# Performance work log

Measured on AMD Instinct MI355X. Metric: run time of the kernel, lower is better.

Reference implementation:

```python
import jax, jax.numpy as jnp
import numpy as np

B, S, H = 4, 4096, 768
NB = 16            # n_blocks (first factor)
BSZ = H // NB      # 48, block size
LN_EPS = 1e-12


def setup_inputs() -> dict:
    key = jax.random.key(0)
    ks = jax.random.split(key, 6)
    hidden_states = jax.random.normal(ks[0], (B, S, H), dtype=jnp.float32)
    # Monarch factors: B1 has NB blocks of (BSZ,BSZ); B2 has BSZ blocks of (NB,NB)
    w1_blocks = jax.random.normal(ks[1], (NB, BSZ, BSZ), dtype=jnp.float32) / np.sqrt(BSZ)
    w2_blocks = jax.random.normal(ks[2], (BSZ, NB, NB), dtype=jnp.float32) / np.sqrt(NB)
    gate_w = jax.random.normal(ks[3], (H, H), dtype=jnp.float32) / np.sqrt(H)
    gate_b = jnp.zeros((H,), dtype=jnp.float32)
    out_w = jax.random.normal(ks[4], (H, H), dtype=jnp.float32) / np.sqrt(H)
    out_b = jnp.zeros((H,), dtype=jnp.float32)
    ln_gamma = jnp.ones((H,), dtype=jnp.float32)
    ln_beta = jnp.zeros((H,), dtype=jnp.float32)
    return {
        "hidden_states": hidden_states,
        "w1_blocks": w1_blocks,
        "w2_blocks": w2_blocks,
        "gate_w": gate_w,
        "gate_b": gate_b,
        "out_w": out_w,
        "out_b": out_b,
        "ln_gamma": ln_gamma,
        "ln_beta": ln_beta,
    }


def _monarch(x, w1, w2):
    # x: [B, S, H]; Monarch product P B2 P B1 applied to last dim.
    b, s, h = x.shape
    y = x.reshape(b, s, NB, BSZ)
    y = jnp.einsum('bski,kij->bskj', y, w1)      # block-diag (NB blocks of BSZxBSZ)
    y = jnp.swapaxes(y, -1, -2)                  # permute: [B,S,BSZ,NB]
    y = jnp.einsum('bsqi,qij->bsqj', y, w2)      # block-diag (BSZ blocks of NBxNB)
    y = jnp.swapaxes(y, -1, -2)                  # permute back: [B,S,NB,BSZ]
    return y.reshape(b, s, h)


def _layernorm(x, gamma, beta, eps):
    mu = jnp.mean(x, axis=-1, keepdims=True)
    var = jnp.mean(jnp.square(x - mu), axis=-1, keepdims=True)
    return (x - mu) * jax.lax.rsqrt(var + eps) * gamma + beta


def reference(hidden_states, w1_blocks, w2_blocks, gate_w, gate_b,
              out_w, out_b, ln_gamma, ln_beta):
    residual = hidden_states
    mixed = _monarch(hidden_states, w1_blocks, w2_blocks)
    gate = jax.nn.sigmoid(hidden_states @ gate_w.T + gate_b)
    h = mixed * gate
    h = h @ out_w.T + out_b
    # dropout is identity in eval / p=0
    return _layernorm(h + residual, ln_gamma, ln_beta, LN_EPS)
```

## Files before the change

kernel.cpp:

```cpp
#include <hip/hip_runtime.h>
#include <hip/hip_bf16.h>
#include <stdint.h>

#define HD 768

typedef __attribute__((ext_vector_type(8))) short bf16x8;
typedef __attribute__((ext_vector_type(4))) float f32x4;

typedef __attribute__((address_space(3))) void lds_void_t;
typedef const __attribute__((address_space(1))) void gbl_void_t;

__device__ inline void gload_lds16(const void* g, void* l) {
  __builtin_amdgcn_global_load_lds((gbl_void_t*)g, (lds_void_t*)l, 16, 0, 0);
}

__device__ inline unsigned short f2bf(float f) {
  union { float f; unsigned int u; } v; v.f = f;
  return (unsigned short)((v.u + 0x7fffu + ((v.u >> 16) & 1u)) >> 16);
}
__device__ inline float bf2f(unsigned short u) {
  union { unsigned int uu; float f; } v; v.uu = ((unsigned int)u) << 16;
  return v.f;
}

#define BAR() asm volatile("s_barrier" ::: "memory")
#define LGKM(N) { asm volatile("s_waitcnt lgkmcnt(" #N ")" ::: "memory"); __builtin_amdgcn_sched_barrier(0); }
#define VMC(N) asm volatile("s_waitcnt vmcnt(" #N ")" ::: "memory")

__global__ void prep_all_kernel(const float* __restrict__ x,
                                const float* __restrict__ gw, const float* __restrict__ ow,
                                const float* __restrict__ w1, const float* __restrict__ w2,
                                unsigned short* __restrict__ xb,
                                unsigned short* __restrict__ Gwb, unsigned short* __restrict__ Lwb,
                                unsigned short* __restrict__ Opk) {
  int bid = blockIdx.x;
  if (bid < 12288) {
    int i = bid * 256 + threadIdx.x;
    float4 v = ((const float4*)x)[i];
    ushort4 o;
    o.x = f2bf(v.x); o.y = f2bf(v.y); o.z = f2bf(v.z); o.w = f2bf(v.w);
    ((ushort4*)xb)[i] = o;
  } else if (bid < 14592) {
    int e = (bid - 12288) * 256 + threadIdx.x;
    Gwb[e] = f2bf(gw[e]);
  } else if (bid < 16896) {
    int e = (bid - 14592) * 256 + threadIdx.x;
    int n = e / 768, m = e - (e / 768) * 768;
    int k = n / 48, q = n - k * 48;
    int i2 = m / 48, ii = m - i2 * 48;
    float v = w1[(i2 * 48 + ii) * 48 + q] * w2[(q * 16 + i2) * 16 + k];
    Lwb[e] = f2bf(v);
  } else {
    int r = (bid - 16896) * 256 + threadIdx.x;
    int lane = r & 63;
    int ks = (r >> 6) % 24;
    int nt = r / (24 * 64);
    int n = nt * 16 + (lane & 15);
    int k = ks * 32 + (lane >> 4) * 8;
    bf16x8 pack;
#pragma unroll
    for (int j = 0; j < 8; ++j) pack[j] = (short)f2bf(ow[(size_t)n * HD + k + j]);
    *(bf16x8*)(Opk + (size_t)r * 8) = pack;
  }
}

__global__ __launch_bounds__(256, 2)
void gatemix_kernel(const unsigned short* __restrict__ xb,
                    const unsigned short* __restrict__ Gwb,
                    const unsigned short* __restrict__ Lwb,
                    const float* __restrict__ gate_b,
                    unsigned short* __restrict__ hb) {
  __shared__ __align__(16) unsigned char lds[81920];
  const int tid = threadIdx.x, lane = tid & 63;
  const int wid = tid >> 6, wm = wid >> 1, wn = wid & 1;
  const int lr = lane & 15, lg = lane >> 4;

  const int b = blockIdx.x;
  const int work = (b & 7) * 128 + (b >> 3);
  const int panel = work >> 3, nwin = work & 7;
  const size_t m0 = (size_t)panel * 128;
  const int n0 = nwin * 96;

  const int r0 = tid >> 3;
  const int sw = ((tid & 7) << 4) ^ ((r0 & 7) << 4);
  const int v0 = (0 * 32 + r0) * 1536 + sw;
  const int v1 = (1 * 32 + r0) * 1536 + sw;
  const int v2 = (2 * 32 + r0) * 1536 + sw;
  const int v3 = (3 * 32 + r0) * 1536 + sw;
  const unsigned char* aS = (const unsigned char*)xb + m0 * 1536;
  const unsigned char* gS = (const unsigned char*)Gwb + (size_t)n0 * 1536;
  const unsigned char* lS = (const unsigned char*)Lwb + (size_t)n0 * 1536;

#define STAGE_A(KT, BUF) { const unsigned char* s = aS + (KT) * 128; \
    gload_lds16(s + v0, lds + (BUF) * 16384 + tid * 16); \
    gload_lds16(s + v1, lds + (BUF) * 16384 + 4096 + tid * 16); \
    gload_lds16(s + v2, lds + (BUF) * 16384 + 8192 + tid * 16); \
    gload_lds16(s + v3, lds + (BUF) * 16384 + 12288 + tid * 16); }
#define STAGE_BG(KT, BUF) { const unsigned char* s = gS + (KT) * 128; \
    gload_lds16(s + v0, lds + 32768 + (BUF) * 12288 + tid * 16); \
    gload_lds16(s + v1, lds + 32768 + (BUF) * 12288 + 4096 + tid * 16); \
    gload_lds16(s + v2, lds + 32768 + (BUF) * 12288 + 8192 + tid * 16); }
#define STAGE_BL(KT, BUF) { const unsigned char* s = lS + (KT) * 128; \
    gload_lds16(s + v0, lds + 57344 + (BUF) * 12288 + tid * 16); \
    gload_lds16(s + v1, lds + 57344 + (BUF) * 12288 + 4096 + tid * 16); \
    gload_lds16(s + v2, lds + 57344 + (BUF) * 12288 + 8192 + tid * 16); }

  const int sx0 = (lg * 16) ^ ((lr & 7) << 4);
  const int sx1 = sx0 ^ 64;
  const unsigned char* baA0 = lds + (wm * 64 + lr) * 128 + sx0;
  const unsigned char* baA1 = lds + (wm * 64 + lr) * 128 + sx1;
  const unsigned char* baG0 = lds + 32768 + (wn * 48 + lr) * 128 + sx0;
  const unsigned char* baG1 = lds + 32768 + (wn * 48 + lr) * 128 + sx1;
  const unsigned char* baL0 = lds + 57344 + (wn * 48 + lr) * 128 + sx0;
  const unsigned char* baL1 = lds + 57344 + (wn * 48 + lr) * 128 + sx1;

  f32x4 accg[4][3], accm[4][3];
#pragma unroll
  for (int mt = 0; mt < 4; ++mt)
#pragma unroll
    for (int nt = 0; nt < 3; ++nt) { accg[mt][nt] = (f32x4){0,0,0,0}; accm[mt][nt] = (f32x4){0,0,0,0}; }

  bf16x8 aA[4], aB[4];
  bf16x8 bG[3], bL[3];

#define RD_AA(BUF) { _Pragma("unroll") for (int mt = 0; mt < 4; ++mt) \
      aA[mt] = *(const bf16x8*)(baA0 + (BUF) * 16384 + mt * 2048); }
#define RD_AB(BUF) { _Pragma("unroll") for (int mt = 0; mt < 4; ++mt) \
      aB[mt] = *(const bf16x8*)(baA1 + (BUF) * 16384 + mt * 2048); }
#define RD_BG0(BUF) { _Pragma("unroll") for (int nt = 0; nt < 3; ++nt) \
      bG[nt] = *(const bf16x8*)(baG0 + (BUF) * 12288 + nt * 2048); }
#define RD_BG1(BUF) { _Pragma("unroll") for (int nt = 0; nt < 3; ++nt) \
      bG[nt] = *(const bf16x8*)(baG1 + (BUF) * 12288 + nt * 2048); }
#define RD_BL0(BUF) { _Pragma("unroll") for (int nt = 0; nt < 3; ++nt) \
      bL[nt] = *(const bf16x8*)(baL0 + (BUF) * 12288 + nt * 2048); }
#define RD_BL1(BUF) { _Pragma("unroll") for (int nt = 0; nt < 3; ++nt) \
      bL[nt] = *(const bf16x8*)(baL1 + (BUF) * 12288 + nt * 2048); }
#define MM(ACC, AR, BR) { __builtin_amdgcn_s_setprio(1); \
    _Pragma("unroll") for (int mt = 0; mt < 4; ++mt) \
    _Pragma("unroll") for (int nt = 0; nt < 3; ++nt) \
      ACC[mt][nt] = __builtin_amdgcn_mfma_f32_16x16x32_bf16(AR[mt], BR[nt], ACC[mt][nt], 0, 0, 0); \
    __builtin_amdgcn_s_setprio(0); }

#define KT_BODY(KT, BUF, STG, VN) { \
    STAGE_BL((KT) + 1, (BUF) ^ 1); \
    RD_BL0(BUF); \
    LGKM(3); MM(accg, aA, bG); \
    RD_AB(BUF); RD_BG1(BUF); \
    LGKM(7); MM(accm, aA, bL); \
    RD_BL1(BUF); \
    LGKM(3); MM(accg, aB, bG); \
    BAR(); \
    if (STG) { STAGE_A((KT) + 2, BUF); STAGE_BG((KT) + 2, BUF); } \
    VMC(VN); \
    BAR(); \
    RD_AA((BUF) ^ 1); RD_BG0((BUF) ^ 1); \
    LGKM(7); MM(accm, aB, bL); }

  STAGE_A(0, 0); STAGE_BG(0, 0); STAGE_BL(0, 0); STAGE_A(1, 1); STAGE_BG(1, 1);
  VMC(7);
  BAR();
  RD_AA(0); RD_BG0(0);

#pragma unroll 1
  for (int kt = 0; kt < 10; kt += 2) {
    KT_BODY(kt, 0, 1, 7);
    KT_BODY(kt + 1, 1, 1, 7);
  }
  KT_BODY(10, 0, 0, 0);
  RD_BL0(1); LGKM(3); MM(accg, aA, bG);
  RD_AB(1); RD_BG1(1); LGKM(7); MM(accm, aA, bL);
  RD_BL1(1); LGKM(3); MM(accg, aB, bG);
  LGKM(0); MM(accm, aB, bL);

#pragma unroll
  for (int nt = 0; nt < 3; ++nt) {
    const int col = n0 + wn * 48 + nt * 16 + lr;
    const float gbv = gate_b[col];
#pragma unroll
    for (int mt = 0; mt < 4; ++mt) {
#pragma unroll
      for (int i = 0; i < 4; ++i) {
        float g = accg[mt][nt][i] + gbv;
        float s = 1.0f / (1.0f + __expf(-g));
        size_t row = m0 + wm * 64 + mt * 16 + lg * 4 + i;
        hb[row * 768 + col] = f2bf(s * accm[mt][nt][i]);
      }
    }
  }
#undef STAGE_A
#undef STAGE_BG
#undef STAGE_BL
#undef RD_AA
#undef RD_AB
#undef RD_BG0
#undef RD_BG1
#undef RD_BL0
#undef RD_BL1
#undef MM
#undef KT_BODY
}

__global__ __launch_bounds__(512, 2)
void out_ln_kernel(const unsigned short* __restrict__ hb,
                   const unsigned short* __restrict__ Opk,
                   const float* __restrict__ out_b,
                   const unsigned short* __restrict__ xb,
                   const float* __restrict__ gamma,
                   const float* __restrict__ beta,
                   float* __restrict__ out) {
  __shared__ __align__(16) unsigned char lds[16384];
  __shared__ float psum[64][8];
  __shared__ float psq[64][8];

  const int tid = threadIdx.x, lane = tid & 63, wid = tid >> 6;
  const int lr = lane & 15, lg = lane >> 4;
  const size_t m0 = (size_t)blockIdx.x * 64;

  const int srow = tid >> 3;
  const unsigned char* aSrc = (const unsigned char*)hb + (m0 + srow) * 1536
                              + (((tid & 7) << 4) ^ ((srow & 7) << 4));
#define STAGE_A(KT, BUF) gload_lds16(aSrc + (KT) * 128, lds + (BUF) * 8192 + tid * 16)

  const unsigned short* bBase = Opk + ((size_t)(wid * 6) * 24 * 64 + lane) * 8;
#define LOAD_B(KT, BR) { _Pragma("unroll") for (int nt = 0; nt < 6; ++nt) { \
      BR[nt * 2 + 0] = *(const bf16x8*)(bBase + nt * 12288 + ((KT) * 2 + 0) * 512); \
      BR[nt * 2 + 1] = *(const bf16x8*)(bBase + nt * 12288 + ((KT) * 2 + 1) * 512); } }

  const int sx0 = (lg * 16) ^ ((lr & 7) << 4);
  const unsigned char* baA0 = lds + lr * 128 + sx0;
  const unsigned char* baA1 = lds + lr * 128 + (sx0 ^ 64);
#define RD_A(BUF) { _Pragma("unroll") for (int mt = 0; mt < 4; ++mt) { \
      aF0[mt] = *(const bf16x8*)(baA0 + (BUF) * 8192 + mt * 2048); \
      aF1[mt] = *(const bf16x8*)(baA1 + (BUF) * 8192 + mt * 2048); } }

#define MM48(BR) { __builtin_amdgcn_s_setprio(1); \
    _Pragma("unroll") for (int mt = 0; mt < 4; ++mt) \
    _Pragma("unroll") for (int nt = 0; nt < 6; ++nt) { \
      acc[mt][nt] = __builtin_amdgcn_mfma_f32_16x16x32_bf16(aF0[mt], BR[nt * 2 + 0], acc[mt][nt], 0, 0, 0); \
      acc[mt][nt] = __builtin_amdgcn_mfma_f32_16x16x32_bf16(aF1[mt], BR[nt * 2 + 1], acc[mt][nt], 0, 0, 0); } \
    __builtin_amdgcn_s_setprio(0); }

  f32x4 acc[4][6];
#pragma unroll
  for (int mt = 0; mt < 4; ++mt)
#pragma unroll
    for (int nt = 0; nt < 6; ++nt) acc[mt][nt] = (f32x4){0, 0, 0, 0};

  bf16x8 aF0[4], aF1[4];
  bf16x8 bP[12], bQ[12];

#define KT_BODY(KT, BUF, BCUR, BNXT, LAST) { \
    if (!(LAST)) { STAGE_A((KT) + 1, (BUF) ^ 1); LOAD_B((KT) + 1, BNXT); } \
    RD_A(BUF); \
    LGKM(0); \
    if (!(LAST)) { VMC(13); } else { VMC(0); } \
    MM48(BCUR); \
    if (!(LAST)) { VMC(12); BAR(); } }

  STAGE_A(0, 0);
  LOAD_B(0, bP);
  VMC(12);
  BAR();

#pragma unroll 1
  for (int kt = 0; kt < 10; kt += 2) {
    KT_BODY(kt, 0, bP, bQ, 0);
    KT_BODY(kt + 1, 1, bQ, bP, 0);
  }
  KT_BODY(10, 0, bP, bQ, 0);
  KT_BODY(11, 1, bQ, bP, 1);

#pragma unroll
  for (int nt = 0; nt < 6; ++nt) {
    const int col = wid * 96 + nt * 16 + lr;
    const float obv = out_b[col];
#pragma unroll
    for (int mt = 0; mt < 4; ++mt) {
#pragma unroll
      for (int i = 0; i < 4; ++i) {
        size_t row = m0 + mt * 16 + lg * 4 + i;
        acc[mt][nt][i] += obv + bf2f(xb[row * 768 + col]);
      }
    }
  }
#pragma unroll
  for (int mt = 0; mt < 4; ++mt) {
#pragma unroll
    for (int i = 0; i < 4; ++i) {
      float s = 0.f, q = 0.f;
#pragma unroll
      for (int nt = 0; nt < 6; ++nt) { float v = acc[mt][nt][i]; s += v; q += v * v; }
#pragma unroll
      for (int off = 8; off >= 1; off >>= 1) {
        s += __shfl_xor(s, off);
        q += __shfl_xor(q, off);
      }
      if (lr == 0) {
        int rl = mt * 16 + lg * 4 + i;
        psum[rl][wid] = s; psq[rl][wid] = q;
      }
    }
  }
  __syncthreads();
#pragma unroll
  for (int mt = 0; mt < 4; ++mt) {
#pragma unroll
    for (int i = 0; i < 4; ++i) {
      int rl = mt * 16 + lg * 4 + i;
      float s = 0.f, q = 0.f;
#pragma unroll
      for (int w = 0; w < 8; ++w) { s += psum[rl][w]; q += psq[rl][w]; }
      float mu = s * (1.0f / 768.0f);
      float var = q * (1.0f / 768.0f) - mu * mu;
      var = var < 0.f ? 0.f : var;
      float rstd = rsqrtf(var + 1e-12f);
      size_t grow = m0 + rl;
#pragma unroll
      for (int nt = 0; nt < 6; ++nt) {
        int col = wid * 96 + nt * 16 + lr;
        out[grow * 768 + col] = (acc[mt][nt][i] - mu) * rstd * gamma[col] + beta[col];
      }
    }
  }
#undef STAGE_A
#undef LOAD_B
#undef RD_A
#undef MM48
#undef KT_BODY
}

extern "C" void kernel_launch(void* const* d_in, const int* in_sizes, int n_in,
                              void* d_out, int out_size, void* d_ws, size_t ws_size,
                              hipStream_t stream) {
  const float* x   = (const float*)d_in[0];
  const float* w1  = (const float*)d_in[1];
  const float* w2  = (const float*)d_in[2];
  const float* gw  = (const float*)d_in[3];
  const float* gb  = (const float*)d_in[4];
  const float* ow  = (const float*)d_in[5];
  const float* ob  = (const float*)d_in[6];
  const float* gam = (const float*)d_in[7];
  const float* bet = (const float*)d_in[8];
  float* out = (float*)d_out;

  char* ws = (char*)d_ws;
  unsigned short* xb  = (unsigned short*)(ws);
  unsigned short* hb  = (unsigned short*)(ws + 25165824);
  unsigned short* Gwb = (unsigned short*)(ws + 50331648);
  unsigned short* Lwb = (unsigned short*)(ws + 51511296);
  unsigned short* Opk = (unsigned short*)(ws + 52690944);

  prep_all_kernel<<<17184, 256, 0, stream>>>(x, gw, ow, w1, w2, xb, Gwb, Lwb, Opk);
  gatemix_kernel<<<1024, 256, 0, stream>>>(xb, Gwb, Lwb, gb, hb);
  out_ln_kernel<<<256, 512, 0, stream>>>(hb, Opk, ob, xb, gam, bet, out);
}
```

Before: 95.27 us.

## Compute Monarch mixing via structured block-diagonal MFMAs instead of dense fused weight

Before this change the two Monarch factors were folded into one dense 768x768 bf16 matrix and multiplied alongside the gate GEMM. A separate monarch_kernel now applies the two block-diagonal factors directly with small zero-padded MFMAs, staging the permute through swizzled LDS, and writes the bf16 mixed result into the output buffer as scratch. The gate GEMM kernel then does a single dense GEMM with a wider 192-column N tile and reads the mixed value in its epilogue. This roughly halves the dense GEMM FLOPs, at the cost of an extra kernel launch and an extra round trip of the mixed activations through global memory.

```diff
diff --git a/kernel.cpp b/kernel.cpp
--- a/kernel.cpp
+++ b/kernel.cpp
@@ -6,6 +6,7 @@
 
 typedef __attribute__((ext_vector_type(8))) short bf16x8;
 typedef __attribute__((ext_vector_type(4))) float f32x4;
+typedef __attribute__((ext_vector_type(4))) unsigned short u16x4;
 
 typedef __attribute__((address_space(3))) void lds_void_t;
 typedef const __attribute__((address_space(1))) void gbl_void_t;
@@ -31,8 +32,10 @@
                                 const float* __restrict__ gw, const float* __restrict__ ow,
                                 const float* __restrict__ w1, const float* __restrict__ w2,
                                 unsigned short* __restrict__ xb,
-                                unsigned short* __restrict__ Gwb, unsigned short* __restrict__ Lwb,
-                                unsigned short* __restrict__ Opk) {
+                                unsigned short* __restrict__ Gwb,
+                                unsigned short* __restrict__ Opk,
+                                unsigned short* __restrict__ w1f,
+                                unsigned short* __restrict__ w2f) {
   int bid = blockIdx.x;
   if (bid < 12288) {
     int i = bid * 256 + threadIdx.x;
@@ -43,15 +46,8 @@
   } else if (bid < 14592) {
     int e = (bid - 12288) * 256 + threadIdx.x;
     Gwb[e] = f2bf(gw[e]);
-  } else if (bid < 16896) {
-    int e = (bid - 14592) * 256 + threadIdx.x;
-    int n = e / 768, m = e - (e / 768) * 768;
-    int k = n / 48, q = n - k * 48;
-    int i2 = m / 48, ii = m - i2 * 48;
-    float v = w1[(i2 * 48 + ii) * 48 + q] * w2[(q * 16 + i2) * 16 + k];
-    Lwb[e] = f2bf(v);
-  } else {
-    int r = (bid - 16896) * 256 + threadIdx.x;
+  } else if (bid < 14880) {
+    int r = (bid - 14592) * 256 + threadIdx.x;
     int lane = r & 63;
     int ks = (r >> 6) % 24;
     int nt = r / (24 * 64);
@@ -61,142 +57,251 @@
 #pragma unroll
     for (int j = 0; j < 8; ++j) pack[j] = (short)f2bf(ow[(size_t)n * HD + k + j]);
     *(bf16x8*)(Opk + (size_t)r * 8) = pack;
+  } else if (bid < 14904) {
+    int e = (bid - 14880) * 256 + threadIdx.x;
+    int lane = e & 63, fi = e >> 6;
+    int ks = fi & 1, nt = (fi >> 1) % 3, k = fi / 6;
+    int lrr = lane & 15, lgg = lane >> 4;
+    int q = nt * 16 + lrr;
+    bf16x8 pack;
+#pragma unroll
+    for (int j = 0; j < 8; ++j) {
+      int kk = ks * 32 + lgg * 8 + j;
+      float v = (kk < 48) ? w1[(k * 48 + kk) * 48 + q] : 0.0f;
+      pack[j] = (short)f2bf(v);
+    }
+    *(bf16x8*)(w1f + (size_t)e * 8) = pack;
+  } else {
+    int e = (bid - 14904) * 256 + threadIdx.x;
+    int lane = e & 63, q = e >> 6;
+    int lrr = lane & 15, lgg = lane >> 4;
+    bf16x8 pack;
+#pragma unroll
+    for (int j = 0; j < 8; ++j) {
+      int kk = lgg * 8 + j;
+      float v = (kk < 16) ? w2[(q * 16 + kk) * 16 + lrr] : 0.0f;
+      pack[j] = (short)f2bf(v);
+    }
+    *(bf16x8*)(w2f + (size_t)e * 8) = pack;
   }
 }
 
 __global__ __launch_bounds__(256, 2)
-void gatemix_kernel(const unsigned short* __restrict__ xb,
-                    const unsigned short* __restrict__ Gwb,
-                    const unsigned short* __restrict__ Lwb,
-                    const float* __restrict__ gate_b,
-                    unsigned short* __restrict__ hb) {
+void monarch_kernel(const unsigned short* __restrict__ xb,
+                    const unsigned short* __restrict__ w1f,
+                    const unsigned short* __restrict__ w2f,
+                    unsigned short* __restrict__ mx) {
+  __shared__ __align__(16) unsigned char zl[49152];
+  const int tid = threadIdx.x, lane = tid & 63, wid = tid >> 6;
+  const int lr = lane & 15, lg = lane >> 4;
+  const size_t m0 = (size_t)blockIdx.x * 32;
+
+#pragma unroll
+  for (int kb = 0; kb < 4; ++kb) {
+    const int k = wid * 4 + kb;
+    const unsigned short* wf = w1f + (size_t)(k * 6) * 512 + lane * 8;
+    bf16x8 b00 = *(const bf16x8*)(wf + 0 * 512);
+    bf16x8 b01 = *(const bf16x8*)(wf + 1 * 512);
+    bf16x8 b10 = *(const bf16x8*)(wf + 2 * 512);
+    bf16x8 b11 = *(const bf16x8*)(wf + 3 * 512);
+    bf16x8 b20 = *(const bf16x8*)(wf + 4 * 512);
+    bf16x8 b21 = *(const bf16x8*)(wf + 5 * 512);
+#pragma unroll
+    for (int mt = 0; mt < 2; ++mt) {
+      const unsigned short* ar = xb + (m0 + mt * 16 + lr) * 768 + k * 48;
+      bf16x8 a0 = *(const bf16x8*)(ar + lg * 8);
+      bf16x8 a1 = (bf16x8){0, 0, 0, 0, 0, 0, 0, 0};
+      if (lg < 2) a1 = *(const bf16x8*)(ar + 32 + lg * 8);
+      f32x4 c0 = {0, 0, 0, 0}, c1 = {0, 0, 0, 0}, c2 = {0, 0, 0, 0};
+      c0 = __builtin_amdgcn_mfma_f32_16x16x32_bf16(a0, b00, c0, 0, 0, 0);
+      c0 = __builtin_amdgcn_mfma_f32_16x16x32_bf16(a1, b01, c0, 0, 0, 0);
+      c1 = __builtin_amdgcn_mfma_f32_16x16x32_bf16(a0, b10, c1, 0, 0, 0);
+      c1 = __builtin_amdgcn_mfma_f32_16x16x32_bf16(a1, b11, c1, 0, 0, 0);
+      c2 = __builtin_amdgcn_mfma_f32_16x16x32_bf16(a0, b20, c2, 0, 0, 0);
+      c2 = __builtin_amdgcn_mfma_f32_16x16x32_bf16(a1, b21, c2, 0, 0, 0);
+#pragma unroll
+      for (int i = 0; i < 4; ++i) {
+        int row = mt * 16 + lg * 4 + i;
+        int base = row * 1536 + k * 2;
+        int swz = (row & 7) << 4;
+        *(unsigned short*)(zl + ((base + (0 * 16 + lr) * 32) ^ swz)) = f2bf(c0[i]);
+        *(unsigned short*)(zl + ((base + (1 * 16 + lr) * 32) ^ swz)) = f2bf(c1[i]);
+        *(unsigned short*)(zl + ((base + (2 * 16 + lr) * 32) ^ swz)) = f2bf(c2[i]);
+      }
+    }
+  }
+  __syncthreads();
+
+  unsigned int upk[2][4][6];
+#pragma unroll
+  for (int qq = 0; qq < 12; ++qq) {
+    const int q = wid * 12 + qq;
+    bf16x8 bw = *(const bf16x8*)(w2f + (size_t)q * 512 + lane * 8);
+#pragma unroll
+    for (int mt = 0; mt < 2; ++mt) {
+      int row = mt * 16 + lr;
+      int off = (row * 1536 + (lg < 2 ? q * 32 + lg * 16 : 0)) ^ ((row & 7) << 4);
+      bf16x8 a = *(const bf16x8*)(zl + off);
+      if (lg >= 2) a = (bf16x8){0, 0, 0, 0, 0, 0, 0, 0};
+      f32x4 c = {0, 0, 0, 0};
+      c = __builtin_amdgcn_mfma_f32_16x16x32_bf16(a, bw, c, 0, 0, 0);
+#pragma unroll
+      for (int i = 0; i < 4; ++i) {
+        unsigned int h = (unsigned int)f2bf(c[i]);
+        if (qq & 1) upk[mt][i][qq >> 1] |= (h << 16);
+        else        upk[mt][i][qq >> 1] = h;
+      }
+    }
+  }
+  __syncthreads();
+
+  const int wq0 = wid * 12;
+#pragma unroll
+  for (int mt = 0; mt < 2; ++mt) {
+#pragma unroll
+    for (int i = 0; i < 4; ++i) {
+      int row = mt * 16 + lg * 4 + i;
+      int base = row * 1536 + lr * 96 + wq0 * 2;
+      int swz = (row & 7) << 4;
+#pragma unroll
+      for (int p = 0; p < 3; ++p) {
+        uint2 v; v.x = upk[mt][i][p * 2]; v.y = upk[mt][i][p * 2 + 1];
+        *(uint2*)(zl + ((base + p * 8) ^ swz)) = v;
+      }
+    }
+  }
+  __syncthreads();
+
+#pragma unroll
+  for (int p = 0; p < 12; ++p) {
+    int id = p * 256 + tid;
+    int row = id / 96, w16 = id % 96;
+    int by = (row * 1536 + w16 * 16) ^ ((row & 7) << 4);
+    f32x4 v = *(const f32x4*)(zl + by);
+    *(f32x4*)((unsigned char*)mx + (m0 + row) * 1536 + w16 * 16) = v;
+  }
+}
+
+__global__ __launch_bounds__(256, 2)
+void gate_mix_kernel(const unsigned short* __restrict__ xb,
+                     const unsigned short* __restrict__ Gwb,
+                     const float* __restrict__ gate_b,
+                     const unsigned short* __restrict__ mx,
+                     unsigned short* __restrict__ hb) {
   __shared__ __align__(16) unsigned char lds[81920];
   const int tid = threadIdx.x, lane = tid & 63;
   const int wid = tid >> 6, wm = wid >> 1, wn = wid & 1;
   const int lr = lane & 15, lg = lane >> 4;
 
   const int b = blockIdx.x;
-  const int work = (b & 7) * 128 + (b >> 3);
-  const int panel = work >> 3, nwin = work & 7;
+  const int work = (b & 7) * 64 + (b >> 3);
+  const int panel = work >> 2, nwin = work & 3;
   const size_t m0 = (size_t)panel * 128;
-  const int n0 = nwin * 96;
+  const int n0 = nwin * 192;
 
   const int r0 = tid >> 3;
   const int sw = ((tid & 7) << 4) ^ ((r0 & 7) << 4);
-  const int v0 = (0 * 32 + r0) * 1536 + sw;
-  const int v1 = (1 * 32 + r0) * 1536 + sw;
-  const int v2 = (2 * 32 + r0) * 1536 + sw;
-  const int v3 = (3 * 32 + r0) * 1536 + sw;
+  const int o0 = (0 * 32 + r0) * 1536 + sw;
+  const int o1 = (1 * 32 + r0) * 1536 + sw;
+  const int o2 = (2 * 32 + r0) * 1536 + sw;
+  const int o3 = (3 * 32 + r0) * 1536 + sw;
+  const int o4 = (4 * 32 + r0) * 1536 + sw;
+  const int o5 = (5 * 32 + r0) * 1536 + sw;
   const unsigned char* aS = (const unsigned char*)xb + m0 * 1536;
-  const unsigned char* gS = (const unsigned char*)Gwb + (size_t)n0 * 1536;
-  const unsigned char* lS = (const unsigned char*)Lwb + (size_t)n0 * 1536;
-
-#define STAGE_A(KT, BUF) { const unsigned char* s = aS + (KT) * 128; \
-    gload_lds16(s + v0, lds + (BUF) * 16384 + tid * 16); \
-    gload_lds16(s + v1, lds + (BUF) * 16384 + 4096 + tid * 16); \
-    gload_lds16(s + v2, lds + (BUF) * 16384 + 8192 + tid * 16); \
-    gload_lds16(s + v3, lds + (BUF) * 16384 + 12288 + tid * 16); }
-#define STAGE_BG(KT, BUF) { const unsigned char* s = gS + (KT) * 128; \
-    gload_lds16(s + v0, lds + 32768 + (BUF) * 12288 + tid * 16); \
-    gload_lds16(s + v1, lds + 32768 + (BUF) * 12288 + 4096 + tid * 16); \
-    gload_lds16(s + v2, lds + 32768 + (BUF) * 12288 + 8192 + tid * 16); }
-#define STAGE_BL(KT, BUF) { const unsigned char* s = lS + (KT) * 128; \
-    gload_lds16(s + v0, lds + 57344 + (BUF) * 12288 + tid * 16); \
-    gload_lds16(s + v1, lds + 57344 + (BUF) * 12288 + 4096 + tid * 16); \
-    gload_lds16(s + v2, lds + 57344 + (BUF) * 12288 + 8192 + tid * 16); }
+  const unsigned char* bS = (const unsigned char*)Gwb + (size_t)n0 * 1536;
+
+#define STAGE_A(KT, BUF) { const unsigned char* sp = aS + (KT) * 128; \
+    gload_lds16(sp + o0, lds + (BUF) * 16384 + tid * 16); \
+    gload_lds16(sp + o1, lds + (BUF) * 16384 + 4096 + tid * 16); \
+    gload_lds16(sp + o2, lds + (BUF) * 16384 + 8192 + tid * 16); \
+    gload_lds16(sp + o3, lds + (BUF) * 16384 + 12288 + tid * 16); }
+#define STAGE_B(KT, BUF) { const unsigned char* sp = bS + (KT) * 128; \
+    gload_lds16(sp + o0, lds + 32768 + (BUF) * 24576 + tid * 16); \
+    gload_lds16(sp + o1, lds + 32768 + (BUF) * 24576 + 4096 + tid * 16); \
+    gload_lds16(sp + o2, lds + 32768 + (BUF) * 24576 + 8192 + tid * 16); \
+    gload_lds16(sp + o3, lds + 32768 + (BUF) * 24576 + 12288 + tid * 16); \
+    gload_lds16(sp + o4, lds + 32768 + (BUF) * 24576 + 16384 + tid * 16); \
+    gload_lds16(sp + o5, lds + 32768 + (BUF) * 24576 + 20480 + tid * 16); }
 
   const int sx0 = (lg * 16) ^ ((lr & 7) << 4);
   const int sx1 = sx0 ^ 64;
   const unsigned char* baA0 = lds + (wm * 64 + lr) * 128 + sx0;
   const unsigned char* baA1 = lds + (wm * 64 + lr) * 128 + sx1;
-  const unsigned char* baG0 = lds + 32768 + (wn * 48 + lr) * 128 + sx0;
-  const unsigned char* baG1 = lds + 32768 + (wn * 48 + lr) * 128 + sx1;
-  const unsigned char* baL0 = lds + 57344 + (wn * 48 + lr) * 128 + sx0;
-  const unsigned char* baL1 = lds + 57344 + (wn * 48 + lr) * 128 + sx1;
-
-  f32x4 accg[4][3], accm[4][3];
+  const unsigned char* baB0 = lds + 32768 + (wn * 96 + lr) * 128 + sx0;
+  const unsigned char* baB1 = lds + 32768 + (wn * 96 + lr) * 128 + sx1;
+
+  f32x4 acc[4][6];
 #pragma unroll
   for (int mt = 0; mt < 4; ++mt)
 #pragma unroll
-    for (int nt = 0; nt < 3; ++nt) { accg[mt][nt] = (f32x4){0,0,0,0}; accm[mt][nt] = (f32x4){0,0,0,0}; }
+    for (int nt = 0; nt < 6; ++nt) acc[mt][nt] = (f32x4){0, 0, 0, 0};
 
   bf16x8 aA[4], aB[4];
-  bf16x8 bG[3], bL[3];
+  bf16x8 bB0[6], bB1[6];
 
 #define RD_AA(BUF) { _Pragma("unroll") for (int mt = 0; mt < 4; ++mt) \
       aA[mt] = *(const bf16x8*)(baA0 + (BUF) * 16384 + mt * 2048); }
 #define RD_AB(BUF) { _Pragma("unroll") for (int mt = 0; mt < 4; ++mt) \
       aB[mt] = *(const bf16x8*)(baA1 + (BUF) * 16384 + mt * 2048); }
-#define RD_BG0(BUF) { _Pragma("unroll") for (int nt = 0; nt < 3; ++nt) \
-      bG[nt] = *(const bf16x8*)(baG0 + (BUF) * 12288 + nt * 2048); }
-#define RD_BG1(BUF) { _Pragma("unroll") for (int nt = 0; nt < 3; ++nt) \
-      bG[nt] = *(const bf16x8*)(baG1 + (BUF) * 12288 + nt * 2048); }
-#define RD_BL0(BUF) { _Pragma("unroll") for (int nt = 0; nt < 3; ++nt) \
-      bL[nt] = *(const bf16x8*)(baL0 + (BUF) * 12288 + nt * 2048); }
-#define RD_BL1(BUF) { _Pragma("unroll") for (int nt = 0; nt < 3; ++nt) \
-      bL[nt] = *(const bf16x8*)(baL1 + (BUF) * 12288 + nt * 2048); }
-#define MM(ACC, AR, BR) { __builtin_amdgcn_s_setprio(1); \
+#define RD_B0(BUF) { _Pragma("unroll") for (int nt = 0; nt < 6; ++nt) \
+      bB0[nt] = *(const bf16x8*)(baB0 + (BUF) * 24576 + nt * 2048); }
+#define RD_B1(BUF) { _Pragma("unroll") for (int nt = 0; nt < 6; ++nt) \
+      bB1[nt] = *(const bf16x8*)(baB1 + (BUF) * 24576 + nt * 2048); }
+#define MM24(AR, BR) { __builtin_amdgcn_s_setprio(1); \
     _Pragma("unroll") for (int mt = 0; mt < 4; ++mt) \
-    _Pragma("unroll") for (int nt = 0; nt < 3; ++nt) \
-      ACC[mt][nt] = __builtin_amdgcn_mfma_f32_16x16x32_bf16(AR[mt], BR[nt], ACC[mt][nt], 0, 0, 0); \
+    _Pragma("unroll") for (int nt = 0; nt < 6; ++nt) \
+      acc[mt][nt] = __builtin_amdgcn_mfma_f32_16x16x32_bf16(AR[mt], BR[nt], acc[mt][nt], 0, 0, 0); \
     __builtin_amdgcn_s_setprio(0); }
 
 #define KT_BODY(KT, BUF, STG, VN) { \
-    STAGE_BL((KT) + 1, (BUF) ^ 1); \
-    RD_BL0(BUF); \
-    LGKM(3); MM(accg, aA, bG); \
-    RD_AB(BUF); RD_BG1(BUF); \
-    LGKM(7); MM(accm, aA, bL); \
-    RD_BL1(BUF); \
-    LGKM(3); MM(accg, aB, bG); \
+    RD_AB(BUF); RD_B1(BUF); \
+    LGKM(10); MM24(aA, bB0); \
+    LGKM(0); \
     BAR(); \
-    if (STG) { STAGE_A((KT) + 2, BUF); STAGE_BG((KT) + 2, BUF); } \
+    if (STG) { STAGE_A((KT) + 2, BUF); STAGE_B((KT) + 2, BUF); } \
     VMC(VN); \
     BAR(); \
-    RD_AA((BUF) ^ 1); RD_BG0((BUF) ^ 1); \
-    LGKM(7); MM(accm, aB, bL); }
-
-  STAGE_A(0, 0); STAGE_BG(0, 0); STAGE_BL(0, 0); STAGE_A(1, 1); STAGE_BG(1, 1);
-  VMC(7);
+    RD_AA((BUF) ^ 1); RD_B0((BUF) ^ 1); \
+    MM24(aB, bB1); }
+
+  STAGE_A(0, 0); STAGE_B(0, 0); STAGE_A(1, 1); STAGE_B(1, 1);
+  VMC(10);
   BAR();
-  RD_AA(0); RD_BG0(0);
+  RD_AA(0); RD_B0(0);
 
 #pragma unroll 1
   for (int kt = 0; kt < 10; kt += 2) {
-    KT_BODY(kt, 0, 1, 7);
-    KT_BODY(kt + 1, 1, 1, 7);
+    KT_BODY(kt, 0, 1, 10);
+    KT_BODY(kt + 1, 1, 1, 10);
   }
   KT_BODY(10, 0, 0, 0);
-  RD_BL0(1); LGKM(3); MM(accg, aA, bG);
-  RD_AB(1); RD_BG1(1); LGKM(7); MM(accm, aA, bL);
-  RD_BL1(1); LGKM(3); MM(accg, aB, bG);
-  LGKM(0); MM(accm, aB, bL);
-
-#pragma unroll
-  for (int nt = 0; nt < 3; ++nt) {
-    const int col = n0 + wn * 48 + nt * 16 + lr;
+  RD_AB(1); RD_B1(1);
+  LGKM(10); MM24(aA, bB0);
+  LGKM(0);  MM24(aB, bB1);
+
+#pragma unroll
+  for (int nt = 0; nt < 6; ++nt) {
+    const int col = n0 + wn * 96 + nt * 16 + lr;
     const float gbv = gate_b[col];
 #pragma unroll
     for (int mt = 0; mt < 4; ++mt) {
 #pragma unroll
       for (int i = 0; i < 4; ++i) {
-        float g = accg[mt][nt][i] + gbv;
+        size_t row = m0 + wm * 64 + mt * 16 + lg * 4 + i;
+        float g = acc[mt][nt][i] + gbv;
         float s = 1.0f / (1.0f + __expf(-g));
-        size_t row = m0 + wm * 64 + mt * 16 + lg * 4 + i;
-        hb[row * 768 + col] = f2bf(s * accm[mt][nt][i]);
+        float mval = bf2f(mx[row * 768 + col]);
+        hb[row * 768 + col] = f2bf(s * mval);
       }
     }
   }
 #undef STAGE_A
-#undef STAGE_BG
-#undef STAGE_BL
+#undef STAGE_B
 #undef RD_AA
 #undef RD_AB
-#undef RD_BG0
-#undef RD_BG1
-#undef RD_BL0
-#undef RD_BL1
-#undef MM
+#undef RD_B0
+#undef RD_B1
+#undef MM24
 #undef KT_BODY
 }
 
@@ -347,10 +452,13 @@
   unsigned short* xb  = (unsigned short*)(ws);
   unsigned short* hb  = (unsigned short*)(ws + 25165824);
   unsigned short* Gwb = (unsigned short*)(ws + 50331648);
-  unsigned short* Lwb = (unsigned short*)(ws + 51511296);
-  unsigned short* Opk = (unsigned short*)(ws + 52690944);
-
-  prep_all_kernel<<<17184, 256, 0, stream>>>(x, gw, ow, w1, w2, xb, Gwb, Lwb, Opk);
-  gatemix_kernel<<<1024, 256, 0, stream>>>(xb, Gwb, Lwb, gb, hb);
+  unsigned short* Opk = (unsigned short*)(ws + 51511296);
+  unsigned short* w1f = (unsigned short*)(ws + 52690944);
+  unsigned short* w2f = (unsigned short*)(ws + 52789248);
+  unsigned short* mx  = (unsigned short*)d_out;
+
+  prep_all_kernel<<<14916, 256, 0, stream>>>(x, gw, ow, w1, w2, xb, Gwb, Opk, w1f, w2f);
+  monarch_kernel<<<512, 256, 0, stream>>>(xb, w1f, w2f, mx);
+  gate_mix_kernel<<<512, 256, 0, stream>>>(xb, Gwb, gb, mx, hb);
   out_ln_kernel<<<256, 512, 0, stream>>>(hb, Opk, ob, xb, gam, bet, out);
 }
```

Result: slower. 98.21 us (+3.1%).
